# Kernel optimization log

Hardware: AMD Instinct MI355X
Metric: run time of the kernel (lower is better)

The kernel has to match this reference:

```python
import jax, jax.numpy as jnp
import numpy as np
from jax import lax

KERNEL = 31
SMOOTH = 0.001
PAD = KERNEL // 2


def _avg_pool2d(x):
    # torch F.avg_pool2d(kernel=31, stride=1, padding=15, count_include_pad=True):
    # sum over 31x31 window with zero padding, then divide by 31*31 always.
    s = lax.reduce_window(
        x, 0.0, lax.add,
        window_dimensions=(1, 1, KERNEL, KERNEL),
        window_strides=(1, 1, 1, 1),
        padding=((0, 0), (0, 0), (PAD, PAD), (PAD, PAD)),
    )
    return s / (KERNEL * KERNEL)


def setup_inputs() -> dict:
    key = jax.random.key(0)
    k1, k2 = jax.random.split(key)
    B, C, H, W = 32, 1, 1024, 1024
    output = jax.random.normal(k1, (B, C, H, W), dtype=jnp.float32)
    target = jax.random.uniform(k2, (B, C, H, W), dtype=jnp.float32)
    return {"output": output, "target": target}


def reference(output, target):
    out = jax.nn.sigmoid(output)
    weight = 1.0 + 5.0 * jnp.abs(_avg_pool2d(target) - target)  # [B,C,H,W]
    inter = jnp.sum(out * target * weight, axis=(2, 3)).reshape(-1, 1)      # [B*C,1]
    mask_sum = jnp.sum((target + out) * weight, axis=(2, 3)).reshape(-1, 1)  # [B*C,1]
    loss = 1.0 - (2.0 * inter + SMOOTH) / (mask_sum + SMOOTH)
    return jnp.mean(loss)
```

## Files before the change

kernel.cpp:

```cpp
#include <hip/hip_runtime.h>
#include <math.h>


namespace {
constexpr int Bn = 32;
constexpr int Hn = 1024;
constexpr int Wn = 1024;
constexpr int Rn = 15;
constexpr int TX = 256;
constexpr int YS = 64;
constexpr int NB = YS / 8;
constexpr int NCOL = TX + 32;
constexpr int PHYSW = (NCOL / 8) * 12;
constexpr float INV_KK = 1.0f / 961.0f;
}

__device__ __forceinline__ int phys(int i) { return i + ((i >> 3) << 2); }

__device__ __forceinline__ float ldcol(const float* p, int y, int col, bool xok) {
    return (xok && (unsigned)y < (unsigned)Hn) ? p[(size_t)y * Wn + col] : 0.0f;
}

__global__ __launch_bounds__(256, 4)
void dice_main(const float* __restrict__ logits, const float* __restrict__ tgt,
               float* __restrict__ acc)
{
    __shared__ __align__(16) float vbuf[8 * PHYSW];
    __shared__ float red[8];

    const int bid = blockIdx.x;
    const int b   = bid >> 6;
    const int rem = bid & 63;
    const int x0  = (rem >> 4) * TX;
    const int y0  = (rem & 15) * YS;
    const int t   = threadIdx.x;

    const float* tb = tgt    + (size_t)b * Hn * Wn;
    const float* ob = logits + (size_t)b * Hn * Wn;

    const int  col0 = x0 - Rn + t;
    const bool has2 = (t < 32);
    const int  col1 = col0 + 256;
    const bool xok0 = (col0 >= 0) && (col0 < Wn);
    const bool xok1 = (col1 >= 0) && (col1 < Wn);
    const int  pt   = phys(t);
    const int  pt2  = phys(256 + t);

    const int rr = t >> 5;
    const int jj = t & 31;
    const int xb = x0 + (jj << 3);

    float vs0 = 0.0f, vs1 = 0.0f;
    for (int yy = y0 - Rn; yy <= y0 + Rn; ++yy) {
        vs0 += ldcol(tb, yy, col0, xok0);
        if (has2) vs1 += ldcol(tb, yy, col1, xok1);
    }

    float pA[8], qA[8];
    #pragma unroll
    for (int r = 0; r < 8; ++r) {
        pA[r] = ldcol(tb, y0 + r + Rn, col0, xok0);
        qA[r] = has2 ? ldcol(tb, y0 + r + Rn, col1, xok1) : 0.0f;
    }
    float4 ct0, ct1, co0, co1;
    {
        const float* tp = tb + (size_t)(y0 + rr) * Wn + xb;
        const float* op = ob + (size_t)(y0 + rr) * Wn + xb;
        ct0 = ((const float4*)tp)[0]; ct1 = ((const float4*)tp)[1];
        co0 = ((const float4*)op)[0]; co1 = ((const float4*)op)[1];
    }

    float acc_i = 0.0f, acc_m = 0.0f;

    for (int it = 0; it < NB; ++it) {
        const int ya = y0 + it * 8;

        #pragma unroll
        for (int r = 0; r < 8; ++r) {
            const int yr = ya + r;
            if (it > 0 || r > 0) {
                vs0 += pA[r] - ldcol(tb, yr - Rn - 1, col0, xok0);
                if (has2) vs1 += qA[r] - ldcol(tb, yr - Rn - 1, col1, xok1);
            }
            vbuf[r * PHYSW + pt] = vs0;
            if (has2) vbuf[r * PHYSW + pt2] = vs1;
        }
        __syncthreads();

        float4 nt0, nt1, no0, no1;
        if (it + 1 < NB) {
            #pragma unroll
            for (int r = 0; r < 8; ++r) {
                pA[r] = ldcol(tb, ya + 8 + r + Rn, col0, xok0);
                if (has2) qA[r] = ldcol(tb, ya + 8 + r + Rn, col1, xok1);
            }
            const float* tp = tb + (size_t)(ya + 8 + rr) * Wn + xb;
            const float* op = ob + (size_t)(ya + 8 + rr) * Wn + xb;
            nt0 = ((const float4*)tp)[0]; nt1 = ((const float4*)tp)[1];
            no0 = ((const float4*)op)[0]; no1 = ((const float4*)op)[1];
        }

        {
            const float* vrow = &vbuf[rr * PHYSW];
            float w[40];
            #pragma unroll
            for (int k = 0; k < 10; ++k) {
                const float4 q = *(const float4*)&vrow[phys((jj << 3) + (k << 2))];
                w[4 * k + 0] = q.x; w[4 * k + 1] = q.y;
                w[4 * k + 2] = q.z; w[4 * k + 3] = q.w;
            }

            const float tc[8] = {ct0.x, ct0.y, ct0.z, ct0.w, ct1.x, ct1.y, ct1.z, ct1.w};
            const float oc[8] = {co0.x, co0.y, co0.z, co0.w, co1.x, co1.y, co1.z, co1.w};

            float s0 = 0.0f, s1 = 0.0f, s2 = 0.0f, s3 = 0.0f;
            #pragma unroll
            for (int c = 0; c < 28; c += 4) {
                s0 += w[c]; s1 += w[c + 1]; s2 += w[c + 2]; s3 += w[c + 3];
            }
            float s = (s0 + s1) + (s2 + s3) + w[28] + w[29] + w[30];
            #pragma unroll
            for (int m = 0; m < 8; ++m) {
                if (m > 0) s += w[30 + m] - w[m - 1];
                const float avg = s * INV_KK;
                const float wt  = 1.0f + 5.0f * fabsf(avg - tc[m]);
                const float sg  = 1.0f / (1.0f + __expf(-oc[m]));
                acc_i += sg * tc[m] * wt;
                acc_m += (tc[m] + sg) * wt;
            }
        }

        if (it + 1 < NB) { ct0 = nt0; ct1 = nt1; co0 = no0; co1 = no1; }
        __syncthreads();
    }

    #pragma unroll
    for (int off = 32; off > 0; off >>= 1) {
        acc_i += __shfl_down(acc_i, off);
        acc_m += __shfl_down(acc_m, off);
    }
    const int lane = t & 63;
    const int wv   = t >> 6;
    if (lane == 0) { red[wv * 2] = acc_i; red[wv * 2 + 1] = acc_m; }
    __syncthreads();
    if (t == 0) {
        atomicAdd(&acc[2 * b],     red[0] + red[2] + red[4] + red[6]);
        atomicAdd(&acc[2 * b + 1], red[1] + red[3] + red[5] + red[7]);
    }
}

__global__ void dice_final(const float* __restrict__ acc, float* __restrict__ out)
{
    const int t = threadIdx.x;
    float l = 0.0f;
    if (t < Bn) {
        const float I = acc[2 * t];
        const float M = acc[2 * t + 1];
        l = 1.0f - (2.0f * I + 0.001f) / (M + 0.001f);
    }
    #pragma unroll
    for (int off = 32; off > 0; off >>= 1) l += __shfl_down(l, off);
    if (t == 0) out[0] = l * (1.0f / 32.0f);
}

extern "C" void kernel_launch(void* const* d_in, const int* in_sizes, int n_in,
                              void* d_out, int out_size, void* d_ws, size_t ws_size,
                              hipStream_t stream)
{
    const float* logits = (const float*)d_in[0];
    const float* target = (const float*)d_in[1];
    float* acc = (float*)d_ws;

    hipMemsetAsync(d_ws, 0, 64 * sizeof(float), stream);
    dice_main<<<dim3(Bn * 64), dim3(256), 0, stream>>>(logits, target, acc);
    dice_final<<<dim3(1), dim3(64), 0, stream>>>(acc, (float*)d_out);
}
```

Before: 338.6 us.

## Stage target rows in a shared-memory ring buffer and enlarge row tiles

Replaces the repeated global reads of target rows (added row, subtracted row, centre row) with a 6-slot shared-memory ring of 8-row groups. Each target element is loaded from global once per block and then reused for the vertical running sum and the centre values. YS grows from 64 to 256, so the grid drops to 512 blocks and the vertical halo is amortised over more rows. The cost is much larger shared memory per block, fewer resident blocks (launch bound 2), and only 512 blocks to fill the GPU.

```diff
diff --git a/kernel.cpp b/kernel.cpp
--- a/kernel.cpp
+++ b/kernel.cpp
@@ -8,66 +8,77 @@
 constexpr int Wn = 1024;
 constexpr int Rn = 15;
 constexpr int TX = 256;
-constexpr int YS = 64;
+constexpr int YS = 256;
 constexpr int NB = YS / 8;
-constexpr int NCOL = TX + 32;
-constexpr int PHYSW = (NCOL / 8) * 12;
+constexpr int SC = 320;
+constexpr int PHYSW = 432;
 constexpr float INV_KK = 1.0f / 961.0f;
 }
 
 __device__ __forceinline__ int phys(int i) { return i + ((i >> 3) << 2); }
-
-__device__ __forceinline__ float ldcol(const float* p, int y, int col, bool xok) {
-    return (xok && (unsigned)y < (unsigned)Hn) ? p[(size_t)y * Wn + col] : 0.0f;
-}
-
-__global__ __launch_bounds__(256, 4)
+__device__ __forceinline__ int rslot(int row) { return ((row + 48) >> 3) % 6; }
+
+__global__ __launch_bounds__(256, 2)
 void dice_main(const float* __restrict__ logits, const float* __restrict__ tgt,
                float* __restrict__ acc)
 {
+    __shared__ __align__(16) float ring[6][8][SC];
     __shared__ __align__(16) float vbuf[8 * PHYSW];
     __shared__ float red[8];
 
     const int bid = blockIdx.x;
-    const int b   = bid >> 6;
-    const int rem = bid & 63;
-    const int x0  = (rem >> 4) * TX;
-    const int y0  = (rem & 15) * YS;
+    const int b   = bid >> 4;
+    const int rem = bid & 15;
+    const int x0  = (rem >> 2) * TX;
+    const int y0  = (rem & 3) * YS;
     const int t   = threadIdx.x;
 
     const float* tb = tgt    + (size_t)b * Hn * Wn;
     const float* ob = logits + (size_t)b * Hn * Wn;
 
-    const int  col0 = x0 - Rn + t;
-    const bool has2 = (t < 32);
-    const int  col1 = col0 + 256;
-    const bool xok0 = (col0 >= 0) && (col0 < Wn);
-    const bool xok1 = (col1 >= 0) && (col1 < Wn);
-    const int  pt   = phys(t);
-    const int  pt2  = phys(256 + t);
+    const bool st2 = (t < 64);
+    const int  cs0 = min(max(x0 - 16 + t, 0), Wn - 1);
+    const int  cs1 = min(max(x0 + 240 + t, 0), Wn - 1);
+
+    const bool  has2 = (t < 32);
+    const float xm0  = (x0 - 15 + t >= 0 && x0 - 15 + t < Wn) ? 1.0f : 0.0f;
+    const float xm1  = (x0 + 241 + t < Wn) ? 1.0f : 0.0f;
+    const int   pt   = phys(t);
+    const int   pt2  = phys(t + 256);
 
     const int rr = t >> 5;
     const int jj = t & 31;
     const int xb = x0 + (jj << 3);
 
+    #pragma unroll
+    for (int gi = 0; gi < 5; ++gi) {
+        const int row0 = y0 - 16 + gi * 8;
+        const int sl   = rslot(row0);
+        #pragma unroll
+        for (int r = 0; r < 8; ++r) {
+            const int row = min(max(row0 + r, 0), Hn - 1);
+            const size_t off = (size_t)row * Wn;
+            ring[sl][r][t] = tb[off + cs0];
+            if (st2) ring[sl][r][t + 256] = tb[off + cs1];
+        }
+    }
+
+    float4 co0, co1;
+    {
+        const float* op = ob + (size_t)(y0 + rr) * Wn + xb;
+        co0 = ((const float4*)op)[0]; co1 = ((const float4*)op)[1];
+    }
+    __syncthreads();
+
     float vs0 = 0.0f, vs1 = 0.0f;
-    for (int yy = y0 - Rn; yy <= y0 + Rn; ++yy) {
-        vs0 += ldcol(tb, yy, col0, xok0);
-        if (has2) vs1 += ldcol(tb, yy, col1, xok1);
-    }
-
-    float pA[8], qA[8];
-    #pragma unroll
-    for (int r = 0; r < 8; ++r) {
-        pA[r] = ldcol(tb, y0 + r + Rn, col0, xok0);
-        qA[r] = has2 ? ldcol(tb, y0 + r + Rn, col1, xok1) : 0.0f;
-    }
-    float4 ct0, ct1, co0, co1;
-    {
-        const float* tp = tb + (size_t)(y0 + rr) * Wn + xb;
-        const float* op = ob + (size_t)(y0 + rr) * Wn + xb;
-        ct0 = ((const float4*)tp)[0]; ct1 = ((const float4*)tp)[1];
-        co0 = ((const float4*)op)[0]; co1 = ((const float4*)op)[1];
+    #pragma unroll
+    for (int yy = -Rn; yy <= Rn; ++yy) {
+        const int row = y0 + yy;
+        const float m = (row >= 0) ? 1.0f : 0.0f;
+        const int sl = rslot(row);
+        const int ri = row & 7;
+        vs0 += m * ring[sl][ri][t + 1];
+        if (has2) vs1 += m * ring[sl][ri][t + 257];
     }
 
     float acc_i = 0.0f, acc_m = 0.0f;
@@ -77,28 +88,40 @@
 
         #pragma unroll
         for (int r = 0; r < 8; ++r) {
-            const int yr = ya + r;
             if (it > 0 || r > 0) {
-                vs0 += pA[r] - ldcol(tb, yr - Rn - 1, col0, xok0);
-                if (has2) vs1 += qA[r] - ldcol(tb, yr - Rn - 1, col1, xok1);
-            }
-            vbuf[r * PHYSW + pt] = vs0;
-            if (has2) vbuf[r * PHYSW + pt2] = vs1;
+                const int rowa = ya + r + Rn;
+                const int rows = ya + r - Rn - 1;
+                const float ma = (rowa < Hn) ? 1.0f : 0.0f;
+                const float ms = (rows >= 0) ? 1.0f : 0.0f;
+                const int sa = rslot(rowa), ia  = rowa & 7;
+                const int ss = rslot(rows), is_ = rows & 7;
+                vs0 += ma * ring[sa][ia][t + 1] - ms * ring[ss][is_][t + 1];
+                if (has2)
+                    vs1 += ma * ring[sa][ia][t + 257] - ms * ring[ss][is_][t + 257];
+            }
+            vbuf[r * PHYSW + pt] = vs0 * xm0;
+            if (has2) vbuf[r * PHYSW + pt2] = vs1 * xm1;
         }
         __syncthreads();
 
-        float4 nt0, nt1, no0, no1;
-        if (it + 1 < NB) {
+        float stA[8], stB[8];
+        float4 no0, no1;
+        const bool more = (it + 1 < NB);
+        if (more) {
             #pragma unroll
             for (int r = 0; r < 8; ++r) {
-                pA[r] = ldcol(tb, ya + 8 + r + Rn, col0, xok0);
-                if (has2) qA[r] = ldcol(tb, ya + 8 + r + Rn, col1, xok1);
-            }
-            const float* tp = tb + (size_t)(ya + 8 + rr) * Wn + xb;
+                const int row = min(ya + 24 + r, Hn - 1);
+                const size_t off = (size_t)row * Wn;
+                stA[r] = tb[off + cs0];
+                if (st2) stB[r] = tb[off + cs1];
+            }
             const float* op = ob + (size_t)(ya + 8 + rr) * Wn + xb;
-            nt0 = ((const float4*)tp)[0]; nt1 = ((const float4*)tp)[1];
             no0 = ((const float4*)op)[0]; no1 = ((const float4*)op)[1];
         }
+
+        const int gt = rslot(ya);
+        const float4 ct0 = *(const float4*)&ring[gt][rr][16 + (jj << 3)];
+        const float4 ct1 = *(const float4*)&ring[gt][rr][20 + (jj << 3)];
 
         {
             const float* vrow = &vbuf[rr * PHYSW];
@@ -130,7 +153,15 @@
             }
         }
 
-        if (it + 1 < NB) { ct0 = nt0; ct1 = nt1; co0 = no0; co1 = no1; }
+        if (more) {
+            const int gs = rslot(ya + 24);
+            #pragma unroll
+            for (int r = 0; r < 8; ++r) {
+                ring[gs][r][t] = stA[r];
+                if (st2) ring[gs][r][t + 256] = stB[r];
+            }
+            co0 = no0; co1 = no1;
+        }
         __syncthreads();
     }
 
@@ -172,6 +203,6 @@
     float* acc = (float*)d_ws;
 
     hipMemsetAsync(d_ws, 0, 64 * sizeof(float), stream);
-    dice_main<<<dim3(Bn * 64), dim3(256), 0, stream>>>(logits, target, acc);
+    dice_main<<<dim3(Bn * 16), dim3(256), 0, stream>>>(logits, target, acc);
     dice_final<<<dim3(1), dim3(64), 0, stream>>>(acc, (float*)d_out);
 }
```

After: 311.4 us. 1.09x faster.
